# Performance work log

Measured on AMD Instinct MI355X. Metric: run time of the kernel, lower is better.

The kernel has to match this reference:

```python
import jax, jax.numpy as jnp
import numpy as np

LN_EPS = 1e-5

def setup_inputs() -> dict:
    key = jax.random.key(0)
    ks = jax.random.split(key, 8)
    B, L, D = 1, 768, 1024
    DP, H, NB = 128, 128, 64
    s = lambda fan_in: 1.0 / np.sqrt(fan_in)
    return {
        "x": jax.random.normal(ks[0], (B, L, D), dtype=jnp.float32),
        "W_down": jax.random.normal(ks[1], (DP, D), dtype=jnp.float32) * s(D),
        "b_down": jax.random.normal(ks[2], (DP,), dtype=jnp.float32) * s(D),
        "W1": jax.random.normal(ks[3], (H, DP), dtype=jnp.float32) * s(DP),
        "b1": jax.random.normal(ks[4], (H,), dtype=jnp.float32) * s(DP),
        "ln_g": jnp.ones((H,), dtype=jnp.float32),
        "ln_b": jnp.zeros((H,), dtype=jnp.float32),
        "W2": jax.random.normal(ks[5], (NB, H), dtype=jnp.float32) * s(H),
        "b2": jax.random.normal(ks[6], (NB,), dtype=jnp.float32) * s(H),
    }

def reference(x, W_down, b_down, W1, b1, ln_g, ln_b, W2, b2):
    # downproject: [B,L,D] -> [B,L,DP]
    xd = jnp.einsum("bld,pd->blp", x, W_down) + b_down
    q, k = jnp.split(xd, 2, axis=-1)                      # each [B,L,DP/2]
    prod = q[:, None, :, :] * k[:, :, None, :]            # [B,L,L,DP/2]
    diff = q[:, None, :, :] - k[:, :, None, :]            # [B,L,L,DP/2]
    h = jnp.concatenate([prod, diff], axis=-1)            # [B,L,L,DP]
    h = jnp.einsum("bijp,hp->bijh", h, W1) + b1           # [B,L,L,H]
    h = jax.nn.gelu(h, approximate=False)                 # torch GELU is exact erf form
    mu = jnp.mean(h, axis=-1, keepdims=True)
    var = jnp.mean(jnp.square(h - mu), axis=-1, keepdims=True)
    h = (h - mu) * jax.lax.rsqrt(var + LN_EPS) * ln_g + ln_b
    out = jnp.einsum("bijh,nh->bijn", h, W2) + b2         # [B,L,L,NB]
    return out
```

## Files before the change

kernel.cpp:

```cpp
#include <hip/hip_runtime.h>
#include <hip/hip_bf16.h>

#define LL 768
#define DD 1024
#define DP 128
#define HP 64
#define HH 128
#define NB 64

typedef float f32x4 __attribute__((ext_vector_type(4)));
typedef __bf16 bf16x8 __attribute__((ext_vector_type(8)));
typedef __bf16 bf16x4 __attribute__((ext_vector_type(4)));

#define GLOAD_LDS16(g, l) __builtin_amdgcn_global_load_lds( \
    (const __attribute__((address_space(1))) void*)(g), \
    (__attribute__((address_space(3))) void*)(l), 16, 0, 0)

__device__ __forceinline__ float gelu_exact(float x) {
    const float z = fabsf(x) * 0.70710678118654752f;
    const float t = __builtin_amdgcn_rcpf(__builtin_fmaf(0.3275911f, z, 1.0f));
    float p = __builtin_fmaf(t, 1.061405429f, -1.453152027f);
    p = __builtin_fmaf(t, p, 1.421413741f);
    p = __builtin_fmaf(t, p, -0.284496736f);
    p = __builtin_fmaf(t, p, 0.254829592f);
    p = p * t;
    const float e = __expf(-z * z);
    const float erfz = __builtin_fmaf(-p, e, 1.0f);
    const float phi = 0.5f * (1.0f + copysignf(erfz, x));
    return x * phi;
}

template<bool EMIT_MIG>
__global__ __launch_bounds__(256) void prep_kernel(
    const float* __restrict__ x, const float* __restrict__ Wd,
    const float* __restrict__ bd, const float* __restrict__ W1,
    const float* __restrict__ b1, const float* __restrict__ W2,
    const float* __restrict__ lng, const float* __restrict__ lnb,
    const float* __restrict__ b2,
    __hip_bfloat16* __restrict__ qb, float* __restrict__ kf,
    float* __restrict__ A2, float* __restrict__ Bv,
    __hip_bfloat16* __restrict__ W2gb, float* __restrict__ c2b,
    __hip_bfloat16* __restrict__ Mig)
{
    __shared__ __align__(16) float xs[4 * DD];
    __shared__ __align__(16) float xdl[4 * 128];
    const int bid  = blockIdx.x;
    const int tid  = threadIdx.x;
    const int w    = tid >> 6;
    const int lane = tid & 63;

    if (bid >= 192) {
        const int nb = bid - 192;
        for (int e = tid; e < 8 * HH; e += 256) {
            const int n = nb * 8 + (e >> 7), h = e & 127;
            W2gb[n * HH + h] = __float2bfloat16(W2[n * HH + h] * lng[h]);
        }
        #pragma unroll
        for (int rr = 0; rr < 2; ++rr) {
            const int n = nb * 8 + w * 2 + rr;
            float s = W2[n * HH + lane] * lnb[lane]
                    + W2[n * HH + 64 + lane] * lnb[64 + lane];
            #pragma unroll
            for (int m = 1; m < 64; m <<= 1) s += __shfl_xor(s, m);
            if (lane == 0) c2b[n] = s + b2[n];
        }
        return;
    }

    const int l0 = bid * 4;
    const float4* xg = (const float4*)(x + (size_t)l0 * DD);
    float4* xs4 = (float4*)xs;
    for (int idx = tid; idx < 4 * DD / 4; idx += 256) xs4[idx] = xg[idx];
    __syncthreads();

    const int p = tid & 127;
    const int rg = tid >> 7;
    float acc[2] = {0.f, 0.f};
    #pragma unroll 8
    for (int c = 0; c < DD; c += 4) {
        float4 wv = *(const float4*)(Wd + (size_t)p * DD + c);
        #pragma unroll
        for (int rr = 0; rr < 2; ++rr) {
            float4 xv = *(const float4*)(xs + (rg * 2 + rr) * DD + c);
            acc[rr] += wv.x * xv.x + wv.y * xv.y + wv.z * xv.z + wv.w * xv.w;
        }
    }
    const float bdp = bd[p];
    #pragma unroll
    for (int rr = 0; rr < 2; ++rr) {
        const int row = rg * 2 + rr;
        const float v = acc[rr] + bdp;
        xdl[row * 128 + p] = v;
        if (p < HP) qb[(size_t)(l0 + row) * HP + p] = __float2bfloat16(v);
        else        kf[(size_t)(l0 + row) * HP + (p - HP)] = v;
    }
    __syncthreads();

    {
        const int h = tid & 127;
        const int sel = tid >> 7;
        float a4[4] = {0.f, 0.f, 0.f, 0.f};
        #pragma unroll
        for (int c = 0; c < HP; c += 4) {
            float4 wv = *(const float4*)(W1 + (size_t)h * DP + HP + c);
            #pragma unroll
            for (int r = 0; r < 4; ++r) {
                float4 xv = *(const float4*)(xdl + r * 128 + (sel ? HP : 0) + c);
                a4[r] += wv.x * xv.x + wv.y * xv.y + wv.z * xv.z + wv.w * xv.w;
            }
        }
        if (sel == 0) {
            const float bb = b1[h];
            #pragma unroll
            for (int r = 0; r < 4; ++r)
                A2[(size_t)(l0 + r) * HH + h] = a4[r] + bb;
        } else {
            #pragma unroll
            for (int r = 0; r < 4; ++r)
                Bv[(size_t)(l0 + r) * HH + h] = a4[r];
        }
    }

    if (EMIT_MIG) {
        const int po = (tid & 7) * 8;
        const int hb = tid >> 3;
        #pragma unroll
        for (int hh = 0; hh < 4; ++hh) {
            const int h = hh * 32 + hb;
            float4 wA = *(const float4*)(W1 + (size_t)h * DP + po);
            float4 wB = *(const float4*)(W1 + (size_t)h * DP + po + 4);
            #pragma unroll
            for (int r = 0; r < 4; ++r) {
                float4 kA = *(const float4*)(xdl + r * 128 + HP + po);
                float4 kB = *(const float4*)(xdl + r * 128 + HP + po + 4);
                bf16x8 t;
                t[0] = (__bf16)(wA.x * kA.x); t[1] = (__bf16)(wA.y * kA.y);
                t[2] = (__bf16)(wA.z * kA.z); t[3] = (__bf16)(wA.w * kA.w);
                t[4] = (__bf16)(wB.x * kB.x); t[5] = (__bf16)(wB.y * kB.y);
                t[6] = (__bf16)(wB.z * kB.z); t[7] = (__bf16)(wB.w * kB.w);
                *(bf16x8*)&Mig[((size_t)(l0 + r) * HH + h) * HP + po] = t;
            }
        }
    }
}

template<bool USE_MIG>
__global__ __launch_bounds__(256, 3) void main_kernel(
    const float* __restrict__ W1, const __hip_bfloat16* __restrict__ W2gb,
    const __hip_bfloat16* __restrict__ qb, const float* __restrict__ kf,
    const float* __restrict__ A2, const float* __restrict__ Bv,
    const float* __restrict__ c2b, const __hip_bfloat16* __restrict__ Mig,
    float* __restrict__ out)
{
    __shared__ __align__(16) unsigned char smem[49152];
    __bf16* Mi   = (__bf16*)smem;
    __bf16* qt   = (__bf16*)(smem + 16384);
    __bf16* W2gs = (__bf16*)(smem + 32768);
    __bf16* hbuf = (__bf16*)smem;

    const int tid  = threadIdx.x;
    const int lane = tid & 63;
    const int w    = tid >> 6;
    const int lo   = lane & 15;
    const int g4   = lane >> 4;
    const int sw   = (lo & 7) << 3;
    const int n    = blockIdx.x;
    const int xcd  = n & 7;
    const int slot = n >> 3;
    const int i    = xcd * 96 + slot / 6;
    const int j0   = (slot % 6) * 128;

    if (USE_MIG) {
        const char* migb = (const char*)Mig + (size_t)i * HH * HP * 2;
        #pragma unroll
        for (int c = 0; c < 4; ++c) {
            const int row = w * 32 + c * 8 + (lane >> 3);
            const int bc  = (lane & 7) * 16;
            const char* src = migb + row * 128 + (bc ^ ((row & 7) << 4));
            GLOAD_LDS16(src, (char*)Mi + w * 4096 + c * 1024);
        }
    } else {
        const int hrow = tid >> 1;
        const int pb = (tid & 1) * 32;
        const int swr = (hrow & 7) << 3;
        const float* w1r = W1 + (size_t)hrow * DP + pb;
        const float* kfr = kf + (size_t)i * HP + pb;
        #pragma unroll
        for (int m = 0; m < 4; ++m) {
            float4 w0 = *(const float4*)(w1r + m * 8);
            float4 w1v = *(const float4*)(w1r + m * 8 + 4);
            float4 k0 = *(const float4*)(kfr + m * 8);
            float4 k1 = *(const float4*)(kfr + m * 8 + 4);
            bf16x8 t;
            t[0] = (__bf16)(w0.x * k0.x); t[1] = (__bf16)(w0.y * k0.y);
            t[2] = (__bf16)(w0.z * k0.z); t[3] = (__bf16)(w0.w * k0.w);
            t[4] = (__bf16)(w1v.x * k1.x); t[5] = (__bf16)(w1v.y * k1.y);
            t[6] = (__bf16)(w1v.z * k1.z); t[7] = (__bf16)(w1v.w * k1.w);
            *(bf16x8*)&Mi[hrow * 64 + ((pb + m * 8) ^ swr)] = t;
        }
    }
    {
        const char* qbb = (const char*)qb + (size_t)j0 * HP * 2;
        #pragma unroll
        for (int c = 0; c < 4; ++c) {
            const int row = w * 32 + c * 8 + (lane >> 3);
            const int bc  = (lane & 7) * 16;
            const char* src = qbb + row * 128 + (bc ^ ((row & 7) << 4));
            GLOAD_LDS16(src, (char*)qt + w * 4096 + c * 1024);
        }
    }
    {
        const char* w2b = (const char*)W2gb;
        #pragma unroll
        for (int c = 0; c < 4; ++c) {
            const int row = w * 16 + c * 4 + (lane >> 4);
            const int bc  = (lane & 15) * 16;
            const char* src = w2b + row * 256 + (bc ^ ((row & 7) << 4));
            GLOAD_LDS16(src, (char*)W2gs + w * 4096 + c * 1024);
        }
    }
    __syncthreads();

    f32x4 acc[2][8];
    #pragma unroll
    for (int a = 0; a < 2; ++a)
        #pragma unroll
        for (int b = 0; b < 8; ++b)
            #pragma unroll
            for (int e = 0; e < 4; ++e) acc[a][b][e] = 0.f;

    #pragma unroll
    for (int kk = 0; kk < 2; ++kk) {
        const int colx = (kk * 32 + g4 * 8) ^ sw;
        bf16x8 bq[2];
        #pragma unroll
        for (int jt = 0; jt < 2; ++jt)
            bq[jt] = *(const bf16x8*)&qt[(32 * w + jt * 16 + lo) * 64 + colx];
        #pragma unroll
        for (int ht = 0; ht < 8; ++ht) {
            bf16x8 am = *(const bf16x8*)&Mi[(ht * 16 + lo) * 64 + colx];
            #pragma unroll
            for (int jt = 0; jt < 2; ++jt)
                acc[jt][ht] = __builtin_amdgcn_mfma_f32_16x16x32_bf16(am, bq[jt], acc[jt][ht], 0, 0, 0);
        }
    }

    __syncthreads();

    #pragma unroll
    for (int jt = 0; jt < 2; ++jt) {
        const int jl = 32 * w + jt * 16 + lo;
        const float* a2r = A2 + (size_t)(j0 + jl) * HH;
        const float* bvr = Bv + (size_t)i * HH;
        float s = 0.f, ss = 0.f;
        #pragma unroll
        for (int ht = 0; ht < 8; ++ht) {
            const int h4 = ht * 16 + g4 * 4;
            f32x4 a2v = *(const f32x4*)&a2r[h4];
            f32x4 bvv = *(const f32x4*)&bvr[h4];
            #pragma unroll
            for (int r = 0; r < 4; ++r) {
                float v = acc[jt][ht][r] + a2v[r] - bvv[r];
                float g = gelu_exact(v);
                acc[jt][ht][r] = g;
                s += g;
                ss = __builtin_fmaf(g, g, ss);
            }
        }
        s  += __shfl_xor(s, 16);  s  += __shfl_xor(s, 32);
        ss += __shfl_xor(ss, 16); ss += __shfl_xor(ss, 32);
        const float mu   = s * (1.0f / 128.0f);
        const float var  = ss * (1.0f / 128.0f) - mu * mu;
        const float rstd = rsqrtf(var + 1e-5f);
        const float nmr  = -mu * rstd;
        #pragma unroll
        for (int ht = 0; ht < 8; ++ht) {
            bf16x4 t;
            #pragma unroll
            for (int r = 0; r < 4; ++r)
                t[r] = (__bf16)__builtin_fmaf(acc[jt][ht][r], rstd, nmr);
            *(bf16x4*)&hbuf[jl * 128 + ((ht * 16 + g4 * 4) ^ sw)] = t;
        }
    }
    asm volatile("s_waitcnt lgkmcnt(0)" ::: "memory");
    __builtin_amdgcn_sched_barrier(0);

    f32x4 acc2[2][4];
    #pragma unroll
    for (int a = 0; a < 2; ++a)
        #pragma unroll
        for (int b = 0; b < 4; ++b)
            #pragma unroll
            for (int e = 0; e < 4; ++e) acc2[a][b][e] = 0.f;

    #pragma unroll
    for (int kk = 0; kk < 4; ++kk) {
        const int colx = (kk * 32 + g4 * 8) ^ sw;
        bf16x8 bh[2];
        #pragma unroll
        for (int jt = 0; jt < 2; ++jt)
            bh[jt] = *(const bf16x8*)&hbuf[(32 * w + jt * 16 + lo) * 128 + colx];
        #pragma unroll
        for (int nt2 = 0; nt2 < 4; ++nt2) {
            bf16x8 aw = *(const bf16x8*)&W2gs[(nt2 * 16 + lo) * 128 + colx];
            #pragma unroll
            for (int jt = 0; jt < 2; ++jt)
                acc2[jt][nt2] = __builtin_amdgcn_mfma_f32_16x16x32_bf16(aw, bh[jt], acc2[jt][nt2], 0, 0, 0);
        }
    }

    #pragma unroll
    for (int jt = 0; jt < 2; ++jt) {
        const int j = j0 + 32 * w + jt * 16 + lo;
        const size_t base = ((size_t)i * LL + j) * NB;
        #pragma unroll
        for (int nt2 = 0; nt2 < 4; ++nt2) {
            const int n4 = nt2 * 16 + g4 * 4;
            f32x4 c2bv = *(const f32x4*)&c2b[n4];
            f32x4 o;
            #pragma unroll
            for (int r = 0; r < 4; ++r)
                o[r] = acc2[jt][nt2][r] + c2bv[r];
            *(f32x4*)&out[base + n4] = o;
        }
    }
}

extern "C" void kernel_launch(void* const* d_in, const int* in_sizes, int n_in,
                              void* d_out, int out_size, void* d_ws, size_t ws_size,
                              hipStream_t stream) {
    const float* x   = (const float*)d_in[0];
    const float* Wd  = (const float*)d_in[1];
    const float* bd  = (const float*)d_in[2];
    const float* W1  = (const float*)d_in[3];
    const float* b1  = (const float*)d_in[4];
    const float* lng = (const float*)d_in[5];
    const float* lnb = (const float*)d_in[6];
    const float* W2  = (const float*)d_in[7];
    const float* b2  = (const float*)d_in[8];
    float* out = (float*)d_out;

    char* ws = (char*)d_ws;
    __hip_bfloat16* qb   = (__hip_bfloat16*)ws;
    float* kf    = (float*)(ws + 98304);
    float* A2    = (float*)(ws + 294912);
    float* Bv    = (float*)(ws + 688128);
    __hip_bfloat16* W2gb = (__hip_bfloat16*)(ws + 1081344);
    float* c2b   = (float*)(ws + 1097728);
    __hip_bfloat16* Mig  = (__hip_bfloat16*)(ws + 1097984);
    const bool useMig = ws_size >= (size_t)1097984 + 12582912;

    if (useMig) {
        prep_kernel<true><<<200, 256, 0, stream>>>(x, Wd, bd, W1, b1, W2, lng,
            lnb, b2, qb, kf, A2, Bv, W2gb, c2b, Mig);
        main_kernel<true><<<4608, 256, 0, stream>>>(W1, W2gb, qb, kf, A2, Bv,
            c2b, Mig, out);
    } else {
        prep_kernel<false><<<200, 256, 0, stream>>>(x, Wd, bd, W1, b1, W2, lng,
            lnb, b2, qb, kf, A2, Bv, W2gb, c2b, Mig);
        main_kernel<false><<<4608, 256, 0, stream>>>(W1, W2gb, qb, kf, A2, Bv,
            c2b, Mig, out);
    }
}
```

Before: 109.6 us.

## Loop each block over three j-tiles to reuse the Mi tile, with per-wave fencing

Each block now covers one i row and three consecutive 128-wide j tiles instead of one, so the grid shrinks from 4608 to 1536 blocks. The Mi and W2 tiles are loaded into LDS once per block rather than once per tile. The hbuf region now aliases each wave's own private qt rows, and GEMM2 runs per 16-row jt slice. That lets per-wave lgkm/vm waits replace the mid-kernel block barrier and lowers accumulator register pressure. The cost is that the next q tile is fetched and waited on right away with no overlap, and fewer blocks give less parallelism to hide latency.

```diff
diff --git a/kernel.cpp b/kernel.cpp
--- a/kernel.cpp
+++ b/kernel.cpp
@@ -15,6 +15,13 @@
 #define GLOAD_LDS16(g, l) __builtin_amdgcn_global_load_lds( \
     (const __attribute__((address_space(1))) void*)(g), \
     (__attribute__((address_space(3))) void*)(l), 16, 0, 0)
+
+#define WAVE_FENCE_LGKM() do { \
+    asm volatile("s_waitcnt lgkmcnt(0)" ::: "memory"); \
+    __builtin_amdgcn_sched_barrier(0); } while (0)
+#define WAVE_FENCE_VM() do { \
+    asm volatile("s_waitcnt vmcnt(0)" ::: "memory"); \
+    __builtin_amdgcn_sched_barrier(0); } while (0)
 
 __device__ __forceinline__ float gelu_exact(float x) {
     const float z = fabsf(x) * 0.70710678118654752f;
@@ -154,9 +161,9 @@
 {
     __shared__ __align__(16) unsigned char smem[49152];
     __bf16* Mi   = (__bf16*)smem;
-    __bf16* qt   = (__bf16*)(smem + 16384);
-    __bf16* W2gs = (__bf16*)(smem + 32768);
-    __bf16* hbuf = (__bf16*)smem;
+    __bf16* W2gs = (__bf16*)(smem + 16384);
+    __bf16* qt   = (__bf16*)(smem + 32768);
+    __bf16* hbuf = (__bf16*)(smem + 32768);
 
     const int tid  = threadIdx.x;
     const int lane = tid & 63;
@@ -167,8 +174,8 @@
     const int n    = blockIdx.x;
     const int xcd  = n & 7;
     const int slot = n >> 3;
-    const int i    = xcd * 96 + slot / 6;
-    const int j0   = (slot % 6) * 128;
+    const int i    = xcd * 96 + (slot >> 1);
+    const int jg   = slot & 1;
 
     if (USE_MIG) {
         const char* migb = (const char*)Mig + (size_t)i * HH * HP * 2;
@@ -176,8 +183,8 @@
         for (int c = 0; c < 4; ++c) {
             const int row = w * 32 + c * 8 + (lane >> 3);
             const int bc  = (lane & 7) * 16;
-            const char* src = migb + row * 128 + (bc ^ ((row & 7) << 4));
-            GLOAD_LDS16(src, (char*)Mi + w * 4096 + c * 1024);
+            GLOAD_LDS16(migb + row * 128 + (bc ^ ((row & 7) << 4)),
+                        (char*)Mi + w * 4096 + c * 1024);
         }
     } else {
         const int hrow = tid >> 1;
@@ -200,128 +207,134 @@
         }
     }
     {
-        const char* qbb = (const char*)qb + (size_t)j0 * HP * 2;
+        const char* w2b = (const char*)W2gb;
+        #pragma unroll
+        for (int c = 0; c < 4; ++c) {
+            const int row = w * 16 + c * 4 + (lane >> 4);
+            const int bc  = (lane & 15) * 16;
+            GLOAD_LDS16(w2b + row * 256 + (bc ^ ((row & 7) << 4)),
+                        (char*)W2gs + w * 4096 + c * 1024);
+        }
+    }
+    {
+        const char* qbb = (const char*)qb + (size_t)(jg * 384) * 128;
         #pragma unroll
         for (int c = 0; c < 4; ++c) {
             const int row = w * 32 + c * 8 + (lane >> 3);
             const int bc  = (lane & 7) * 16;
-            const char* src = qbb + row * 128 + (bc ^ ((row & 7) << 4));
-            GLOAD_LDS16(src, (char*)qt + w * 4096 + c * 1024);
-        }
-    }
-    {
-        const char* w2b = (const char*)W2gb;
-        #pragma unroll
-        for (int c = 0; c < 4; ++c) {
-            const int row = w * 16 + c * 4 + (lane >> 4);
-            const int bc  = (lane & 15) * 16;
-            const char* src = w2b + row * 256 + (bc ^ ((row & 7) << 4));
-            GLOAD_LDS16(src, (char*)W2gs + w * 4096 + c * 1024);
+            GLOAD_LDS16(qbb + row * 128 + (bc ^ ((row & 7) << 4)),
+                        (char*)qt + w * 4096 + c * 1024);
         }
     }
     __syncthreads();
 
-    f32x4 acc[2][8];
-    #pragma unroll
-    for (int a = 0; a < 2; ++a)
-        #pragma unroll
-        for (int b = 0; b < 8; ++b)
-            #pragma unroll
-            for (int e = 0; e < 4; ++e) acc[a][b][e] = 0.f;
-
-    #pragma unroll
-    for (int kk = 0; kk < 2; ++kk) {
-        const int colx = (kk * 32 + g4 * 8) ^ sw;
-        bf16x8 bq[2];
-        #pragma unroll
-        for (int jt = 0; jt < 2; ++jt)
-            bq[jt] = *(const bf16x8*)&qt[(32 * w + jt * 16 + lo) * 64 + colx];
-        #pragma unroll
-        for (int ht = 0; ht < 8; ++ht) {
-            bf16x8 am = *(const bf16x8*)&Mi[(ht * 16 + lo) * 64 + colx];
+    const float* bvr = Bv + (size_t)i * HH;
+
+    for (int t = 0; t < 3; ++t) {
+        const int j0 = jg * 384 + t * 128;
+
+        f32x4 acc[2][8];
+        #pragma unroll
+        for (int a = 0; a < 2; ++a)
+            #pragma unroll
+            for (int b = 0; b < 8; ++b)
+                #pragma unroll
+                for (int e = 0; e < 4; ++e) acc[a][b][e] = 0.f;
+
+        #pragma unroll
+        for (int kk = 0; kk < 2; ++kk) {
+            const int colx = (kk * 32 + g4 * 8) ^ sw;
+            bf16x8 bq[2];
             #pragma unroll
             for (int jt = 0; jt < 2; ++jt)
-                acc[jt][ht] = __builtin_amdgcn_mfma_f32_16x16x32_bf16(am, bq[jt], acc[jt][ht], 0, 0, 0);
-        }
-    }
-
-    __syncthreads();
-
-    #pragma unroll
-    for (int jt = 0; jt < 2; ++jt) {
-        const int jl = 32 * w + jt * 16 + lo;
-        const float* a2r = A2 + (size_t)(j0 + jl) * HH;
-        const float* bvr = Bv + (size_t)i * HH;
-        float s = 0.f, ss = 0.f;
-        #pragma unroll
-        for (int ht = 0; ht < 8; ++ht) {
-            const int h4 = ht * 16 + g4 * 4;
-            f32x4 a2v = *(const f32x4*)&a2r[h4];
-            f32x4 bvv = *(const f32x4*)&bvr[h4];
-            #pragma unroll
-            for (int r = 0; r < 4; ++r) {
-                float v = acc[jt][ht][r] + a2v[r] - bvv[r];
-                float g = gelu_exact(v);
-                acc[jt][ht][r] = g;
-                s += g;
-                ss = __builtin_fmaf(g, g, ss);
-            }
-        }
-        s  += __shfl_xor(s, 16);  s  += __shfl_xor(s, 32);
-        ss += __shfl_xor(ss, 16); ss += __shfl_xor(ss, 32);
-        const float mu   = s * (1.0f / 128.0f);
-        const float var  = ss * (1.0f / 128.0f) - mu * mu;
-        const float rstd = rsqrtf(var + 1e-5f);
-        const float nmr  = -mu * rstd;
-        #pragma unroll
-        for (int ht = 0; ht < 8; ++ht) {
-            bf16x4 t;
-            #pragma unroll
-            for (int r = 0; r < 4; ++r)
-                t[r] = (__bf16)__builtin_fmaf(acc[jt][ht][r], rstd, nmr);
-            *(bf16x4*)&hbuf[jl * 128 + ((ht * 16 + g4 * 4) ^ sw)] = t;
-        }
-    }
-    asm volatile("s_waitcnt lgkmcnt(0)" ::: "memory");
-    __builtin_amdgcn_sched_barrier(0);
-
-    f32x4 acc2[2][4];
-    #pragma unroll
-    for (int a = 0; a < 2; ++a)
-        #pragma unroll
-        for (int b = 0; b < 4; ++b)
-            #pragma unroll
-            for (int e = 0; e < 4; ++e) acc2[a][b][e] = 0.f;
-
-    #pragma unroll
-    for (int kk = 0; kk < 4; ++kk) {
-        const int colx = (kk * 32 + g4 * 8) ^ sw;
-        bf16x8 bh[2];
-        #pragma unroll
-        for (int jt = 0; jt < 2; ++jt)
-            bh[jt] = *(const bf16x8*)&hbuf[(32 * w + jt * 16 + lo) * 128 + colx];
-        #pragma unroll
-        for (int nt2 = 0; nt2 < 4; ++nt2) {
-            bf16x8 aw = *(const bf16x8*)&W2gs[(nt2 * 16 + lo) * 128 + colx];
-            #pragma unroll
-            for (int jt = 0; jt < 2; ++jt)
-                acc2[jt][nt2] = __builtin_amdgcn_mfma_f32_16x16x32_bf16(aw, bh[jt], acc2[jt][nt2], 0, 0, 0);
-        }
-    }
-
-    #pragma unroll
-    for (int jt = 0; jt < 2; ++jt) {
-        const int j = j0 + 32 * w + jt * 16 + lo;
-        const size_t base = ((size_t)i * LL + j) * NB;
-        #pragma unroll
-        for (int nt2 = 0; nt2 < 4; ++nt2) {
-            const int n4 = nt2 * 16 + g4 * 4;
-            f32x4 c2bv = *(const f32x4*)&c2b[n4];
-            f32x4 o;
-            #pragma unroll
-            for (int r = 0; r < 4; ++r)
-                o[r] = acc2[jt][nt2][r] + c2bv[r];
-            *(f32x4*)&out[base + n4] = o;
+                bq[jt] = *(const bf16x8*)&qt[(32 * w + jt * 16 + lo) * 64 + colx];
+            #pragma unroll
+            for (int ht = 0; ht < 8; ++ht) {
+                bf16x8 am = *(const bf16x8*)&Mi[(ht * 16 + lo) * 64 + colx];
+                #pragma unroll
+                for (int jt = 0; jt < 2; ++jt)
+                    acc[jt][ht] = __builtin_amdgcn_mfma_f32_16x16x32_bf16(am, bq[jt], acc[jt][ht], 0, 0, 0);
+            }
+        }
+
+        #pragma unroll
+        for (int jt = 0; jt < 2; ++jt) {
+            const int jl = 32 * w + jt * 16 + lo;
+            const float* a2r = A2 + (size_t)(j0 + jl) * HH;
+            float s = 0.f, ss = 0.f;
+            #pragma unroll
+            for (int ht = 0; ht < 8; ++ht) {
+                const int h4 = ht * 16 + g4 * 4;
+                f32x4 a2v = *(const f32x4*)&a2r[h4];
+                f32x4 bvv = *(const f32x4*)&bvr[h4];
+                #pragma unroll
+                for (int r = 0; r < 4; ++r) {
+                    float v = acc[jt][ht][r] + a2v[r] - bvv[r];
+                    float g = gelu_exact(v);
+                    acc[jt][ht][r] = g;
+                    s += g;
+                    ss = __builtin_fmaf(g, g, ss);
+                }
+            }
+            s  += __shfl_xor(s, 16);  s  += __shfl_xor(s, 32);
+            ss += __shfl_xor(ss, 16); ss += __shfl_xor(ss, 32);
+            const float mu   = s * (1.0f / 128.0f);
+            const float var  = ss * (1.0f / 128.0f) - mu * mu;
+            const float rstd = rsqrtf(var + 1e-5f);
+            const float nmr  = -mu * rstd;
+            const int hrow = w * 16 + lo;
+            #pragma unroll
+            for (int ht = 0; ht < 8; ++ht) {
+                bf16x4 tv;
+                #pragma unroll
+                for (int r = 0; r < 4; ++r)
+                    tv[r] = (__bf16)__builtin_fmaf(acc[jt][ht][r], rstd, nmr);
+                *(bf16x4*)&hbuf[hrow * 128 + ((ht * 16 + g4 * 4) ^ sw)] = tv;
+            }
+            WAVE_FENCE_LGKM();
+
+            f32x4 acc2[4];
+            #pragma unroll
+            for (int b = 0; b < 4; ++b)
+                #pragma unroll
+                for (int e = 0; e < 4; ++e) acc2[b][e] = 0.f;
+
+            #pragma unroll
+            for (int kk = 0; kk < 4; ++kk) {
+                const int colx = (kk * 32 + g4 * 8) ^ sw;
+                bf16x8 bh = *(const bf16x8*)&hbuf[(w * 16 + lo) * 128 + colx];
+                #pragma unroll
+                for (int nt2 = 0; nt2 < 4; ++nt2) {
+                    bf16x8 aw = *(const bf16x8*)&W2gs[(nt2 * 16 + lo) * 128 + colx];
+                    acc2[nt2] = __builtin_amdgcn_mfma_f32_16x16x32_bf16(aw, bh, acc2[nt2], 0, 0, 0);
+                }
+            }
+
+            const int j = j0 + jl;
+            const size_t base = ((size_t)i * LL + j) * NB;
+            #pragma unroll
+            for (int nt2 = 0; nt2 < 4; ++nt2) {
+                const int n4 = nt2 * 16 + g4 * 4;
+                f32x4 c2bv = *(const f32x4*)&c2b[n4];
+                f32x4 o;
+                #pragma unroll
+                for (int r = 0; r < 4; ++r)
+                    o[r] = acc2[nt2][r] + c2bv[r];
+                *(f32x4*)&out[base + n4] = o;
+            }
+            WAVE_FENCE_LGKM();
+        }
+
+        if (t < 2) {
+            const char* qbb = (const char*)qb + (size_t)(j0 + 128) * 128;
+            #pragma unroll
+            for (int c = 0; c < 4; ++c) {
+                const int row = w * 32 + c * 8 + (lane >> 3);
+                const int bc  = (lane & 7) * 16;
+                GLOAD_LDS16(qbb + row * 128 + (bc ^ ((row & 7) << 4)),
+                            (char*)qt + w * 4096 + c * 1024);
+            }
+            WAVE_FENCE_VM();
         }
     }
 }
@@ -353,12 +366,12 @@
     if (useMig) {
         prep_kernel<true><<<200, 256, 0, stream>>>(x, Wd, bd, W1, b1, W2, lng,
             lnb, b2, qb, kf, A2, Bv, W2gb, c2b, Mig);
-        main_kernel<true><<<4608, 256, 0, stream>>>(W1, W2gb, qb, kf, A2, Bv,
+        main_kernel<true><<<1536, 256, 0, stream>>>(W1, W2gb, qb, kf, A2, Bv,
             c2b, Mig, out);
     } else {
         prep_kernel<false><<<200, 256, 0, stream>>>(x, Wd, bd, W1, b1, W2, lng,
             lnb, b2, qb, kf, A2, Bv, W2gb, c2b, Mig);
-        main_kernel<false><<<4608, 256, 0, stream>>>(W1, W2gb, qb, kf, A2, Bv,
+        main_kernel<false><<<1536, 256, 0, stream>>>(W1, W2gb, qb, kf, A2, Bv,
             c2b, Mig, out);
     }
 }
```

After: 119.1 us. +8.6%, slower.
